# Optimization experiments

Measured on AMD Instinct MI355X. Metric: run time of the kernel, lower is better.

## Reference

```python
import jax, jax.numpy as jnp
from jax import lax
import numpy as np

B, T, C = 8, 16384, 64
NUM_FILTERS, FILTER_SIZE = 64, 5
LEAKY_SLOPE = 0.3  # keras activation 'leaky_relu' default negative_slope


def setup_inputs() -> dict:
    key = jax.random.key(0)
    k1, k2, k3 = jax.random.split(key, 3)
    x = jax.random.normal(k1, (B, T, C), dtype=jnp.float32)
    interp_weights = jax.random.normal(k2, (C,), dtype=jnp.float32)
    # Conv1D kernel layout: [filter_size, in_channels, out_channels]
    conv_kernel = jax.random.normal(k3, (FILTER_SIZE, C, NUM_FILTERS), dtype=jnp.float32) * 0.05
    conv_bias = jnp.zeros((NUM_FILTERS,), dtype=jnp.float32)
    return {"x": x, "interp_weights": interp_weights,
            "conv_kernel": conv_kernel, "conv_bias": conv_bias}


def reference(x, interp_weights, conv_kernel, conv_bias):
    # Sigmoid gate per channel
    w = jax.nn.sigmoid(interp_weights)  # [C]
    # The diag conv2d (filter [1,2,C,C], SAME) is: blend[t] = w*x[t] + (1-w)*x[t+1]
    # (TF SAME for even width pads one zero frame on the right)
    x_next = jnp.concatenate([x[:, 1:, :], jnp.zeros_like(x[:, :1, :])], axis=1)
    blend = w * x + (1.0 - w) * x_next  # [B, T, C]
    # Interleave: even positions original, odd positions blended -> [B, 2T, C]
    up = jnp.stack([x, blend], axis=2).reshape(B, 2 * T, C)
    # Conv1D(num_filters, filter_size, padding='same', stride 1) + leaky_relu
    y = lax.conv_general_dilated(
        up, conv_kernel,
        window_strides=(1,), padding='SAME',
        dimension_numbers=('NWC', 'WIO', 'NWC'))
    y = y + conv_bias
    return jnp.where(y >= 0, y, LEAKY_SLOPE * y)
```

## Files before the change

### kernel.cpp

```cpp
#include <hip/hip_runtime.h>
#include <hip/hip_bf16.h>
#include <cstdint>


#define T_ 16384
#define TWO_T 32768
#define XSTRIDE 72
#define WSL 1376

typedef __bf16 bf16x8 __attribute__((ext_vector_type(8)));
typedef __bf16 bf16x4 __attribute__((ext_vector_type(4)));
typedef float  f32x4  __attribute__((ext_vector_type(4)));
typedef unsigned short u16x8 __attribute__((ext_vector_type(8)));

__device__ __forceinline__ float sigmoidf_(float z) {
    return 1.0f / (1.0f + expf(-z));
}

__device__ __forceinline__ unsigned short f2bf(float f) {
    union { float f; uint32_t u; } v; v.f = f;
    uint32_t u = v.u;
    return (unsigned short)((u + 0x7FFFu + ((u >> 16) & 1u)) >> 16);
}

__global__ void lu_prep_kernel(const float* __restrict__ iw,
                               const float* __restrict__ ck,
                               const float* __restrict__ x,
                               unsigned short* __restrict__ bp,
                               float* __restrict__ corrf) {
    int fi = blockIdx.x;
    int l  = threadIdx.x;
    if (fi < 56) {
        int phase, ks, nt;
        if (fi < 24) { phase = 0; ks = fi >> 2; nt = fi & 3; }
        else         { phase = 1; ks = (fi - 24) >> 2; nt = (fi - 24) & 3; }
        int tap = ks >> 1;
        int n   = nt * 16 + (l & 15);
        int c0  = ((ks & 1) << 5) + ((l >> 4) << 3);
        u16x8 pk;
#pragma unroll
        for (int i = 0; i < 8; ++i) {
            int c = c0 + i;
            float w = sigmoidf_(iw[c]);
            float v;
            #define CK(k) ck[((k) * 64 + c) * 64 + n]
            if (phase == 0) {
                if (tap == 0)      v = CK(0) + w * CK(1);
                else if (tap == 1) v = (1.f - w) * CK(1) + CK(2) + w * CK(3);
                else               v = (1.f - w) * CK(3) + CK(4);
            } else {
                if (tap == 0)      v = w * CK(0);
                else if (tap == 1) v = (1.f - w) * CK(0) + CK(1) + w * CK(2);
                else if (tap == 2) v = (1.f - w) * CK(2) + CK(3) + w * CK(4);
                else               v = (1.f - w) * CK(4);
            }
            #undef CK
            pk[i] = f2bf(v);
        }
        *(u16x8*)(bp + (((size_t)fi * 64) + l) * 8) = pk;
    } else {
        int b = fi - 56;
        int f = l;
        float cE = 0.f, cO = 0.f;
#pragma unroll
        for (int c = 0; c < 64; ++c) {
            float w = sigmoidf_(iw[c]);
            float g = (1.f - w) * x[(size_t)b * T_ * 64 + c];
            cE += ck[(64 + c) * 64 + f] * g;
            cO += ck[c * 64 + f] * g;
        }
        corrf[b * 128 + f]      = cE;
        corrf[b * 128 + 64 + f] = cO;
    }
}

__device__ __forceinline__ void issue_loads(const float* __restrict__ x,
                                            int b, int t0, int lane, float4* ld) {
#pragma unroll
    for (int it = 0; it < 5; ++it) {
        int idx = it * 64 + lane;
        int j   = idx >> 4;
        int c4  = (idx & 15) << 2;
        int gf  = t0 - 1 + j;
        float4 v = make_float4(0.f, 0.f, 0.f, 0.f);
        if (idx < 304 && gf >= 0 && gf < T_)
            v = *(const float4*)(x + ((size_t)b * T_ + gf) * 64 + c4);
        ld[it] = v;
    }
}

__global__ __launch_bounds__(256, 4) void lu_main_kernel(
        const float* __restrict__ x,
        const unsigned short* __restrict__ bp,
        const float* __restrict__ corrf,
        const float* __restrict__ bias,
        float* __restrict__ out) {
    __shared__ __align__(16) unsigned short xl[4][WSL];

    const int bid  = blockIdx.x;
    const int b    = bid >> 8;
    const int p0   = (bid & 255) << 6;
    const int tid  = threadIdx.x;
    const int lane = tid & 63;
    const int wv   = tid >> 6;

    unsigned short* xw = &xl[wv][0];

    float4 ld[5];
    issue_loads(x, b, p0, lane, ld);

    bf16x8 We[6], Wo[8];
#pragma unroll
    for (int ks = 0; ks < 6; ++ks)
        We[ks] = __builtin_bit_cast(bf16x8,
            *(const u16x8*)(bp + (((size_t)(ks * 4 + wv)) * 64 + lane) * 8));
#pragma unroll
    for (int ks = 0; ks < 8; ++ks)
        Wo[ks] = __builtin_bit_cast(bf16x8,
            *(const u16x8*)(bp + (((size_t)(24 + ks * 4 + wv)) * 64 + lane) * 8));

    const int hi  = lane >> 4;
    const int col = lane & 15;
    const float4 bias4 = *(const float4*)(bias + (wv << 4) + (hi << 2));

    for (int w = 0; w < 4; ++w) {
        const int t0 = p0 + (w << 4);

#pragma unroll
        for (int it = 0; it < 5; ++it) {
            int idx = it * 64 + lane;
            if (idx < 304) {
                int j  = idx >> 4;
                int c4 = (idx & 15) << 2;
                bf16x4 pk;
                pk[0] = (__bf16)ld[it].x; pk[1] = (__bf16)ld[it].y;
                pk[2] = (__bf16)ld[it].z; pk[3] = (__bf16)ld[it].w;
                *(bf16x4*)(xw + j * XSTRIDE + c4) = pk;
            }
        }

        if (w < 3) issue_loads(x, b, p0 + ((w + 1) << 4), lane, ld);

        f32x4 accE = {0.f, 0.f, 0.f, 0.f};
        f32x4 accO = {0.f, 0.f, 0.f, 0.f};
#pragma unroll
        for (int tap = 0; tap < 4; ++tap)
#pragma unroll
            for (int h = 0; h < 2; ++h) {
                bf16x8 xb = __builtin_bit_cast(bf16x8,
                    *(const u16x8*)(xw + (col + tap) * XSTRIDE + (h << 5) + (hi << 3)));
                int ks = tap * 2 + h;
                if (tap < 3)
                    accE = __builtin_amdgcn_mfma_f32_16x16x32_bf16(We[ks], xb, accE, 0, 0, 0);
                accO = __builtin_amdgcn_mfma_f32_16x16x32_bf16(Wo[ks], xb, accO, 0, 0, 0);
            }

        if (((bid & 255) | w) == 0 && col == 0) {
            const float4 cE4 = *(const float4*)(corrf + b * 128 + (wv << 4) + (hi << 2));
            const float4 cO4 = *(const float4*)(corrf + b * 128 + 64 + (wv << 4) + (hi << 2));
            accE[0] -= cE4.x; accE[1] -= cE4.y; accE[2] -= cE4.z; accE[3] -= cE4.w;
            accO[0] -= cO4.x; accO[1] -= cO4.y; accO[2] -= cO4.z; accO[3] -= cO4.w;
        }

        const int tl = t0 + col;
        const size_t fbase = ((size_t)b * TWO_T + ((size_t)tl << 1)) * 64
                           + (wv << 4) + (hi << 2);
        float4 vE, vO;
        {
            float e0 = accE[0] + bias4.x, e1 = accE[1] + bias4.y,
                  e2 = accE[2] + bias4.z, e3 = accE[3] + bias4.w;
            vE.x = e0 >= 0.f ? e0 : 0.3f * e0;
            vE.y = e1 >= 0.f ? e1 : 0.3f * e1;
            vE.z = e2 >= 0.f ? e2 : 0.3f * e2;
            vE.w = e3 >= 0.f ? e3 : 0.3f * e3;
            float o0 = accO[0] + bias4.x, o1 = accO[1] + bias4.y,
                  o2 = accO[2] + bias4.z, o3 = accO[3] + bias4.w;
            vO.x = o0 >= 0.f ? o0 : 0.3f * o0;
            vO.y = o1 >= 0.f ? o1 : 0.3f * o1;
            vO.z = o2 >= 0.f ? o2 : 0.3f * o2;
            vO.w = o3 >= 0.f ? o3 : 0.3f * o3;
        }
        *(float4*)(out + fbase)      = vE;
        *(float4*)(out + fbase + 64) = vO;
    }
}

extern "C" void kernel_launch(void* const* d_in, const int* in_sizes, int n_in,
                              void* d_out, int out_size, void* d_ws, size_t ws_size,
                              hipStream_t stream) {
    (void)in_sizes; (void)n_in; (void)out_size; (void)ws_size;
    const float* x    = (const float*)d_in[0];
    const float* iw   = (const float*)d_in[1];
    const float* ck   = (const float*)d_in[2];
    const float* bias = (const float*)d_in[3];
    float* out = (float*)d_out;
    unsigned short* bp = (unsigned short*)d_ws;
    float* corrf = (float*)((char*)d_ws + 57344);

    lu_prep_kernel<<<64, 64, 0, stream>>>(iw, ck, x, bp, corrf);
    lu_main_kernel<<<2048, 256, 0, stream>>>(x, bp, corrf, bias, out);
}
```

Before: 34.53 us.

## Use LDS ring buffer with double-buffered prefetch and larger per-block tiles

Each wave now keeps a 32-row circular LDS buffer of bf16 x rows. Only the 16 new rows per step are loaded and converted, instead of reloading the 19-row halo window every step. Loads are double-buffered two steps ahead, and each block handles 128 time steps rather than 64, so the grid is halved. This cuts redundant global loads and conversions and gives more latency hiding, but uses more registers and leaves half as many blocks to spread across the GPU.

```diff
diff --git a/kernel.cpp b/kernel.cpp
--- a/kernel.cpp
+++ b/kernel.cpp
@@ -6,7 +6,7 @@
 #define T_ 16384
 #define TWO_T 32768
 #define XSTRIDE 72
-#define WSL 1376
+#define RING 32
 
 typedef __bf16 bf16x8 __attribute__((ext_vector_type(8)));
 typedef __bf16 bf16x4 __attribute__((ext_vector_type(4)));
@@ -74,18 +74,18 @@
     }
 }
 
-__device__ __forceinline__ void issue_loads(const float* __restrict__ x,
-                                            int b, int t0, int lane, float4* ld) {
-#pragma unroll
-    for (int it = 0; it < 5; ++it) {
-        int idx = it * 64 + lane;
+__device__ __forceinline__ void issue16(const float* __restrict__ xb,
+                                        int f0, int lane, float4* ld) {
+#pragma unroll
+    for (int i = 0; i < 4; ++i) {
+        int idx = i * 64 + lane;
         int j   = idx >> 4;
         int c4  = (idx & 15) << 2;
-        int gf  = t0 - 1 + j;
+        int gf  = f0 + j;
         float4 v = make_float4(0.f, 0.f, 0.f, 0.f);
-        if (idx < 304 && gf >= 0 && gf < T_)
-            v = *(const float4*)(x + ((size_t)b * T_ + gf) * 64 + c4);
-        ld[it] = v;
+        if (gf < T_)
+            v = *(const float4*)(xb + (size_t)gf * 64 + c4);
+        ld[i] = v;
     }
 }
 
@@ -95,19 +95,28 @@
         const float* __restrict__ corrf,
         const float* __restrict__ bias,
         float* __restrict__ out) {
-    __shared__ __align__(16) unsigned short xl[4][WSL];
+    __shared__ __align__(16) unsigned short xl[4][RING * XSTRIDE];
 
     const int bid  = blockIdx.x;
-    const int b    = bid >> 8;
-    const int p0   = (bid & 255) << 6;
-    const int tid  = threadIdx.x;
-    const int lane = tid & 63;
-    const int wv   = tid >> 6;
+    const int b    = bid >> 7;
+    const int q    = bid & 127;
+    const int p0   = q << 7;
+    const int lane = threadIdx.x & 63;
+    const int wv   = threadIdx.x >> 6;
 
     unsigned short* xw = &xl[wv][0];
-
-    float4 ld[5];
-    issue_loads(x, b, p0, lane, ld);
+    const float* xb = x + (size_t)b * T_ * 64;
+
+    float4 pro = make_float4(0.f, 0.f, 0.f, 0.f);
+    {
+        int j = lane >> 4, c4 = (lane & 15) << 2;
+        int gf = p0 - 1 + j;
+        if (lane < 48 && gf >= 0)
+            pro = *(const float4*)(xb + (size_t)gf * 64 + c4);
+    }
+    float4 ldb[2][4];
+    issue16(xb, p0 + 2,  lane, ldb[0]);
+    issue16(xb, p0 + 18, lane, ldb[1]);
 
     bf16x8 We[6], Wo[8];
 #pragma unroll
@@ -123,46 +132,57 @@
     const int col = lane & 15;
     const float4 bias4 = *(const float4*)(bias + (wv << 4) + (hi << 2));
 
-    for (int w = 0; w < 4; ++w) {
-        const int t0 = p0 + (w << 4);
-
-#pragma unroll
-        for (int it = 0; it < 5; ++it) {
-            int idx = it * 64 + lane;
-            if (idx < 304) {
-                int j  = idx >> 4;
-                int c4 = (idx & 15) << 2;
-                bf16x4 pk;
-                pk[0] = (__bf16)ld[it].x; pk[1] = (__bf16)ld[it].y;
-                pk[2] = (__bf16)ld[it].z; pk[3] = (__bf16)ld[it].w;
-                *(bf16x4*)(xw + j * XSTRIDE + c4) = pk;
-            }
-        }
-
-        if (w < 3) issue_loads(x, b, p0 + ((w + 1) << 4), lane, ld);
+    if (lane < 48) {
+        int j = lane >> 4, c4 = (lane & 15) << 2;
+        int r = (j + 31) & 31;
+        bf16x4 pk;
+        pk[0] = (__bf16)pro.x; pk[1] = (__bf16)pro.y;
+        pk[2] = (__bf16)pro.z; pk[3] = (__bf16)pro.w;
+        *(bf16x4*)(xw + r * XSTRIDE + c4) = pk;
+    }
+
+#pragma unroll
+    for (int w = 0; w < 8; ++w) {
+        const int par = w & 1;
+
+#pragma unroll
+        for (int i = 0; i < 4; ++i) {
+            int idx = i * 64 + lane;
+            int j   = idx >> 4;
+            int c4  = (idx & 15) << 2;
+            int r   = (16 * w + 2 + j) & 31;
+            bf16x4 pk;
+            pk[0] = (__bf16)ldb[par][i].x; pk[1] = (__bf16)ldb[par][i].y;
+            pk[2] = (__bf16)ldb[par][i].z; pk[3] = (__bf16)ldb[par][i].w;
+            *(bf16x4*)(xw + r * XSTRIDE + c4) = pk;
+        }
+
+        if (w < 6) issue16(xb, p0 + 16 * (w + 2) + 2, lane, ldb[par]);
 
         f32x4 accE = {0.f, 0.f, 0.f, 0.f};
         f32x4 accO = {0.f, 0.f, 0.f, 0.f};
 #pragma unroll
-        for (int tap = 0; tap < 4; ++tap)
+        for (int tap = 0; tap < 4; ++tap) {
+            const int r = (16 * w - 1 + col + tap) & 31;
 #pragma unroll
             for (int h = 0; h < 2; ++h) {
-                bf16x8 xb = __builtin_bit_cast(bf16x8,
-                    *(const u16x8*)(xw + (col + tap) * XSTRIDE + (h << 5) + (hi << 3)));
+                bf16x8 xfr = __builtin_bit_cast(bf16x8,
+                    *(const u16x8*)(xw + r * XSTRIDE + (h << 5) + (hi << 3)));
                 int ks = tap * 2 + h;
                 if (tap < 3)
-                    accE = __builtin_amdgcn_mfma_f32_16x16x32_bf16(We[ks], xb, accE, 0, 0, 0);
-                accO = __builtin_amdgcn_mfma_f32_16x16x32_bf16(Wo[ks], xb, accO, 0, 0, 0);
+                    accE = __builtin_amdgcn_mfma_f32_16x16x32_bf16(We[ks], xfr, accE, 0, 0, 0);
+                accO = __builtin_amdgcn_mfma_f32_16x16x32_bf16(Wo[ks], xfr, accO, 0, 0, 0);
             }
-
-        if (((bid & 255) | w) == 0 && col == 0) {
+        }
+
+        if (((q | w) == 0) && col == 0) {
             const float4 cE4 = *(const float4*)(corrf + b * 128 + (wv << 4) + (hi << 2));
             const float4 cO4 = *(const float4*)(corrf + b * 128 + 64 + (wv << 4) + (hi << 2));
             accE[0] -= cE4.x; accE[1] -= cE4.y; accE[2] -= cE4.z; accE[3] -= cE4.w;
             accO[0] -= cO4.x; accO[1] -= cO4.y; accO[2] -= cO4.z; accO[3] -= cO4.w;
         }
 
-        const int tl = t0 + col;
+        const int tl = p0 + (w << 4) + col;
         const size_t fbase = ((size_t)b * TWO_T + ((size_t)tl << 1)) * 64
                            + (wv << 4) + (hi << 2);
         float4 vE, vO;
@@ -198,5 +218,5 @@
     float* corrf = (float*)((char*)d_ws + 57344);
 
     lu_prep_kernel<<<64, 64, 0, stream>>>(iw, ck, x, bp, corrf);
-    lu_main_kernel<<<2048, 256, 0, stream>>>(x, bp, corrf, bias, out);
-}
+    lu_main_kernel<<<1024, 256, 0, stream>>>(x, bp, corrf, bias, out);
+}
```

Result: slower. 53.42 us (+54.7%).

## Stage input frames via direct global-to-LDS loads into swizzled fp32 ring buffer

Applied to the files above, without the earlier changes.

Replaces the register-staged load, bf16 convert and LDS write with global_load_lds DMA into a per-wave fp32 ring buffer using an XOR swizzle, with explicit vmcnt waits to overlap later loads with the MFMA work. Out-of-range frames read from a zeroed workspace page instead of being predicated. The bf16 conversion moves to after the LDS read, so LDS traffic doubles and the hand-tuned vmcnt counts depend on exact instruction ordering, which risks stalls or races.

```diff
diff --git a/kernel.cpp b/kernel.cpp
--- a/kernel.cpp
+++ b/kernel.cpp
@@ -5,11 +5,9 @@
 
 #define T_ 16384
 #define TWO_T 32768
-#define XSTRIDE 72
-#define WSL 1376
+#define RING 40
 
 typedef __bf16 bf16x8 __attribute__((ext_vector_type(8)));
-typedef __bf16 bf16x4 __attribute__((ext_vector_type(4)));
 typedef float  f32x4  __attribute__((ext_vector_type(4)));
 typedef unsigned short u16x8 __attribute__((ext_vector_type(8)));
 
@@ -27,7 +25,8 @@
                                const float* __restrict__ ck,
                                const float* __restrict__ x,
                                unsigned short* __restrict__ bp,
-                               float* __restrict__ corrf) {
+                               float* __restrict__ corrf,
+                               float* __restrict__ zp) {
     int fi = blockIdx.x;
     int l  = threadIdx.x;
     if (fi < 56) {
@@ -71,22 +70,35 @@
         }
         corrf[b * 128 + f]      = cE;
         corrf[b * 128 + 64 + f] = cO;
+        if (fi == 63) zp[l] = 0.f;
     }
 }
 
-__device__ __forceinline__ void issue_loads(const float* __restrict__ x,
-                                            int b, int t0, int lane, float4* ld) {
-#pragma unroll
-    for (int it = 0; it < 5; ++it) {
-        int idx = it * 64 + lane;
-        int j   = idx >> 4;
-        int c4  = (idx & 15) << 2;
-        int gf  = t0 - 1 + j;
-        float4 v = make_float4(0.f, 0.f, 0.f, 0.f);
-        if (idx < 304 && gf >= 0 && gf < T_)
-            v = *(const float4*)(x + ((size_t)b * T_ + gf) * 64 + c4);
-        ld[it] = v;
-    }
+__device__ __forceinline__ void gload16(const float* g, float* l) {
+    __builtin_amdgcn_global_load_lds(
+        (const __attribute__((address_space(1))) uint32_t*)g,
+        (__attribute__((address_space(3))) uint32_t*)l, 16, 0, 0);
+}
+
+__device__ __forceinline__ void stage4(const float* __restrict__ xb,
+                                       const float* __restrict__ zp,
+                                       int p0, int S, int lane, float* xw) {
+    int fr = S + (lane >> 4);
+    int f  = p0 + fr - 1;
+    int ch = (lane & 15) ^ ((fr - 1) & 7);
+    const float* gp = ((unsigned)f < (unsigned)T_)
+                    ? xb + ((size_t)f << 6) + (ch << 2)
+                    : zp + (ch << 2);
+    gload16(gp, xw + ((S % RING) << 6));
+}
+
+__device__ __forceinline__ bf16x8 pack8(f32x4 a, f32x4 b) {
+    bf16x8 r;
+    r[0] = (__bf16)a[0]; r[1] = (__bf16)a[1];
+    r[2] = (__bf16)a[2]; r[3] = (__bf16)a[3];
+    r[4] = (__bf16)b[0]; r[5] = (__bf16)b[1];
+    r[6] = (__bf16)b[2]; r[7] = (__bf16)b[3];
+    return r;
 }
 
 __global__ __launch_bounds__(256, 4) void lu_main_kernel(
@@ -94,20 +106,19 @@
         const unsigned short* __restrict__ bp,
         const float* __restrict__ corrf,
         const float* __restrict__ bias,
+        const float* __restrict__ zp,
         float* __restrict__ out) {
-    __shared__ __align__(16) unsigned short xl[4][WSL];
+    __shared__ __align__(16) float xl[4][RING * 64];
 
     const int bid  = blockIdx.x;
     const int b    = bid >> 8;
-    const int p0   = (bid & 255) << 6;
-    const int tid  = threadIdx.x;
-    const int lane = tid & 63;
-    const int wv   = tid >> 6;
-
-    unsigned short* xw = &xl[wv][0];
-
-    float4 ld[5];
-    issue_loads(x, b, p0, lane, ld);
+    const int q    = bid & 255;
+    const int p0   = q << 6;
+    const int lane = threadIdx.x & 63;
+    const int wv   = threadIdx.x >> 6;
+
+    float* xw = &xl[wv][0];
+    const float* xb = x + (size_t)b * T_ * 64;
 
     bf16x8 We[6], Wo[8];
 #pragma unroll
@@ -119,50 +130,58 @@
         Wo[ks] = __builtin_bit_cast(bf16x8,
             *(const u16x8*)(bp + (((size_t)(24 + ks * 4 + wv)) * 64 + lane) * 8));
 
-    const int hi  = lane >> 4;
-    const int col = lane & 15;
+    const int hi   = lane >> 4;
+    const int hi2  = hi << 1;
+    const int col  = lane & 15;
     const float4 bias4 = *(const float4*)(bias + (wv << 4) + (hi << 2));
-
+    const char* xwb = (const char*)xw;
+
+#pragma unroll
+    for (int k = 0; k < 5; ++k) stage4(xb, zp, p0, k * 4, lane, xw);
+
+#pragma unroll
     for (int w = 0; w < 4; ++w) {
-        const int t0 = p0 + (w << 4);
-
-#pragma unroll
-        for (int it = 0; it < 5; ++it) {
-            int idx = it * 64 + lane;
-            if (idx < 304) {
-                int j  = idx >> 4;
-                int c4 = (idx & 15) << 2;
-                bf16x4 pk;
-                pk[0] = (__bf16)ld[it].x; pk[1] = (__bf16)ld[it].y;
-                pk[2] = (__bf16)ld[it].z; pk[3] = (__bf16)ld[it].w;
-                *(bf16x4*)(xw + j * XSTRIDE + c4) = pk;
-            }
-        }
-
-        if (w < 3) issue_loads(x, b, p0 + ((w + 1) << 4), lane, ld);
+        if (w < 3) {
+#pragma unroll
+            for (int k = 0; k < 4; ++k)
+                stage4(xb, zp, p0, 20 + (w << 4) + (k << 2), lane, xw);
+        }
+
+        if (w == 0)      asm volatile("s_waitcnt vmcnt(4)" ::: "memory");
+        else if (w < 3)  asm volatile("s_waitcnt vmcnt(6)" ::: "memory");
+        else             asm volatile("s_waitcnt vmcnt(2)" ::: "memory");
+        __builtin_amdgcn_sched_barrier(0);
 
         f32x4 accE = {0.f, 0.f, 0.f, 0.f};
         f32x4 accO = {0.f, 0.f, 0.f, 0.f};
 #pragma unroll
-        for (int tap = 0; tap < 4; ++tap)
-#pragma unroll
-            for (int h = 0; h < 2; ++h) {
-                bf16x8 xb = __builtin_bit_cast(bf16x8,
-                    *(const u16x8*)(xw + (col + tap) * XSTRIDE + (h << 5) + (hi << 3)));
-                int ks = tap * 2 + h;
-                if (tap < 3)
-                    accE = __builtin_amdgcn_mfma_f32_16x16x32_bf16(We[ks], xb, accE, 0, 0, 0);
-                accO = __builtin_amdgcn_mfma_f32_16x16x32_bf16(Wo[ks], xb, accO, 0, 0, 0);
+        for (int tap = 0; tap < 4; ++tap) {
+            int fr  = (w << 4) + col + tap;
+            int row = fr - (fr >= RING ? RING : 0);
+            int key = (fr - 1) & 7;
+            int off0 = (row << 8) + ((hi2 ^ key) << 4);
+            f32x4 qa = *(const f32x4*)(xwb + off0);
+            f32x4 qb = *(const f32x4*)(xwb + (off0 ^ 16));
+            f32x4 qc = *(const f32x4*)(xwb + off0 + 128);
+            f32x4 qd = *(const f32x4*)(xwb + ((off0 + 128) ^ 16));
+            bf16x8 x0 = pack8(qa, qb);
+            bf16x8 x1 = pack8(qc, qd);
+            if (tap < 3) {
+                accE = __builtin_amdgcn_mfma_f32_16x16x32_bf16(We[tap * 2],     x0, accE, 0, 0, 0);
+                accE = __builtin_amdgcn_mfma_f32_16x16x32_bf16(We[tap * 2 + 1], x1, accE, 0, 0, 0);
             }
-
-        if (((bid & 255) | w) == 0 && col == 0) {
+            accO = __builtin_amdgcn_mfma_f32_16x16x32_bf16(Wo[tap * 2],     x0, accO, 0, 0, 0);
+            accO = __builtin_amdgcn_mfma_f32_16x16x32_bf16(Wo[tap * 2 + 1], x1, accO, 0, 0, 0);
+        }
+
+        if (((q | w) == 0) && col == 0) {
             const float4 cE4 = *(const float4*)(corrf + b * 128 + (wv << 4) + (hi << 2));
             const float4 cO4 = *(const float4*)(corrf + b * 128 + 64 + (wv << 4) + (hi << 2));
             accE[0] -= cE4.x; accE[1] -= cE4.y; accE[2] -= cE4.z; accE[3] -= cE4.w;
             accO[0] -= cO4.x; accO[1] -= cO4.y; accO[2] -= cO4.z; accO[3] -= cO4.w;
         }
 
-        const int tl = t0 + col;
+        const int tl = p0 + (w << 4) + col;
         const size_t fbase = ((size_t)b * TWO_T + ((size_t)tl << 1)) * 64
                            + (wv << 4) + (hi << 2);
         float4 vE, vO;
@@ -196,7 +215,8 @@
     float* out = (float*)d_out;
     unsigned short* bp = (unsigned short*)d_ws;
     float* corrf = (float*)((char*)d_ws + 57344);
-
-    lu_prep_kernel<<<64, 64, 0, stream>>>(iw, ck, x, bp, corrf);
-    lu_main_kernel<<<2048, 256, 0, stream>>>(x, bp, corrf, bias, out);
-}
+    float* zp    = (float*)((char*)d_ws + 61440);
+
+    lu_prep_kernel<<<64, 64, 0, stream>>>(iw, ck, x, bp, corrf, zp);
+    lu_main_kernel<<<2048, 256, 0, stream>>>(x, bp, corrf, bias, zp, out);
+}
```

After: 33.22 us. -3.8%, faster.

## Share one LDS tile of x across all waves, reload weights per step

Applied to the files above, without the earlier changes.

Before, each wave staged its own overlapping 19-frame window of x per 16-step chunk, with software-prefetched loads into registers. Now the whole block cooperatively loads and converts a single 67-frame bf16 tile into shared memory once, followed by one barrier. The per-wave weight fragments are no longer held in registers across iterations; they are reloaded from global/L1 inside each step, with an asm barrier to stop hoisting. Occupancy is raised to 8 blocks per CU. This removes redundant halo loads and register pressure, at the cost of losing load/compute overlap and adding repeated weight reads from cache.

```diff
diff --git a/kernel.cpp b/kernel.cpp
--- a/kernel.cpp
+++ b/kernel.cpp
@@ -5,8 +5,8 @@
 
 #define T_ 16384
 #define TWO_T 32768
+#define NFR 67
 #define XSTRIDE 72
-#define WSL 1376
 
 typedef __bf16 bf16x8 __attribute__((ext_vector_type(8)));
 typedef __bf16 bf16x4 __attribute__((ext_vector_type(4)));
@@ -74,95 +74,84 @@
     }
 }
 
-__device__ __forceinline__ void issue_loads(const float* __restrict__ x,
-                                            int b, int t0, int lane, float4* ld) {
-#pragma unroll
-    for (int it = 0; it < 5; ++it) {
-        int idx = it * 64 + lane;
-        int j   = idx >> 4;
-        int c4  = (idx & 15) << 2;
-        int gf  = t0 - 1 + j;
-        float4 v = make_float4(0.f, 0.f, 0.f, 0.f);
-        if (idx < 304 && gf >= 0 && gf < T_)
-            v = *(const float4*)(x + ((size_t)b * T_ + gf) * 64 + c4);
-        ld[it] = v;
-    }
-}
-
-__global__ __launch_bounds__(256, 4) void lu_main_kernel(
+__global__ __launch_bounds__(256, 8) void lu_main_kernel(
         const float* __restrict__ x,
         const unsigned short* __restrict__ bp,
         const float* __restrict__ corrf,
         const float* __restrict__ bias,
         float* __restrict__ out) {
-    __shared__ __align__(16) unsigned short xl[4][WSL];
+    __shared__ __align__(16) unsigned short xl[NFR * XSTRIDE];
 
     const int bid  = blockIdx.x;
     const int b    = bid >> 8;
-    const int p0   = (bid & 255) << 6;
+    const int q    = bid & 255;
+    const int p0   = q << 6;
     const int tid  = threadIdx.x;
     const int lane = tid & 63;
     const int wv   = tid >> 6;
 
-    unsigned short* xw = &xl[wv][0];
+    const float* xb = x + (size_t)b * T_ * 64;
 
-    float4 ld[5];
-    issue_loads(x, b, p0, lane, ld);
-
-    bf16x8 We[6], Wo[8];
 #pragma unroll
-    for (int ks = 0; ks < 6; ++ks)
-        We[ks] = __builtin_bit_cast(bf16x8,
-            *(const u16x8*)(bp + (((size_t)(ks * 4 + wv)) * 64 + lane) * 8));
-#pragma unroll
-    for (int ks = 0; ks < 8; ++ks)
-        Wo[ks] = __builtin_bit_cast(bf16x8,
-            *(const u16x8*)(bp + (((size_t)(24 + ks * 4 + wv)) * 64 + lane) * 8));
+    for (int it = 0; it < 5; ++it) {
+        int idx = it * 256 + tid;
+        if (idx < NFR * 16) {
+            int j  = idx >> 4;
+            int c4 = (idx & 15) << 2;
+            int gf = p0 - 1 + j;
+            float4 v = make_float4(0.f, 0.f, 0.f, 0.f);
+            if ((unsigned)gf < (unsigned)T_)
+                v = *(const float4*)(xb + ((size_t)gf << 6) + c4);
+            bf16x4 pk;
+            pk[0] = (__bf16)v.x; pk[1] = (__bf16)v.y;
+            pk[2] = (__bf16)v.z; pk[3] = (__bf16)v.w;
+            *(bf16x4*)(xl + j * XSTRIDE + c4) = pk;
+        }
+    }
 
     const int hi  = lane >> 4;
     const int col = lane & 15;
     const float4 bias4 = *(const float4*)(bias + (wv << 4) + (hi << 2));
 
+    __syncthreads();
+
+#pragma unroll 1
     for (int w = 0; w < 4; ++w) {
-        const int t0 = p0 + (w << 4);
-
-#pragma unroll
-        for (int it = 0; it < 5; ++it) {
-            int idx = it * 64 + lane;
-            if (idx < 304) {
-                int j  = idx >> 4;
-                int c4 = (idx & 15) << 2;
-                bf16x4 pk;
-                pk[0] = (__bf16)ld[it].x; pk[1] = (__bf16)ld[it].y;
-                pk[2] = (__bf16)ld[it].z; pk[3] = (__bf16)ld[it].w;
-                *(bf16x4*)(xw + j * XSTRIDE + c4) = pk;
-            }
-        }
-
-        if (w < 3) issue_loads(x, b, p0 + ((w + 1) << 4), lane, ld);
+        uint64_t bpa = (uint64_t)bp;
+        asm("" : "+v"(bpa));
+        const unsigned short* bpw = (const unsigned short*)bpa;
 
         f32x4 accE = {0.f, 0.f, 0.f, 0.f};
         f32x4 accO = {0.f, 0.f, 0.f, 0.f};
 #pragma unroll
-        for (int tap = 0; tap < 4; ++tap)
-#pragma unroll
-            for (int h = 0; h < 2; ++h) {
-                bf16x8 xb = __builtin_bit_cast(bf16x8,
-                    *(const u16x8*)(xw + (col + tap) * XSTRIDE + (h << 5) + (hi << 3)));
-                int ks = tap * 2 + h;
-                if (tap < 3)
-                    accE = __builtin_amdgcn_mfma_f32_16x16x32_bf16(We[ks], xb, accE, 0, 0, 0);
-                accO = __builtin_amdgcn_mfma_f32_16x16x32_bf16(Wo[ks], xb, accO, 0, 0, 0);
+        for (int tap = 0; tap < 4; ++tap) {
+            int r = (w << 4) + col + tap;
+            bf16x8 x0 = __builtin_bit_cast(bf16x8,
+                *(const u16x8*)(xl + r * XSTRIDE + (hi << 3)));
+            bf16x8 x1 = __builtin_bit_cast(bf16x8,
+                *(const u16x8*)(xl + r * XSTRIDE + 32 + (hi << 3)));
+            const size_t f0 = (size_t)(((tap * 2) * 4 + wv) * 64 + lane) * 8;
+            const size_t f1 = (size_t)(((tap * 2 + 1) * 4 + wv) * 64 + lane) * 8;
+            if (tap < 3) {
+                bf16x8 we0 = __builtin_bit_cast(bf16x8, *(const u16x8*)(bpw + f0));
+                bf16x8 we1 = __builtin_bit_cast(bf16x8, *(const u16x8*)(bpw + f1));
+                accE = __builtin_amdgcn_mfma_f32_16x16x32_bf16(we0, x0, accE, 0, 0, 0);
+                accE = __builtin_amdgcn_mfma_f32_16x16x32_bf16(we1, x1, accE, 0, 0, 0);
             }
+            bf16x8 wo0 = __builtin_bit_cast(bf16x8, *(const u16x8*)(bpw + f0 + 12288));
+            bf16x8 wo1 = __builtin_bit_cast(bf16x8, *(const u16x8*)(bpw + f1 + 12288));
+            accO = __builtin_amdgcn_mfma_f32_16x16x32_bf16(wo0, x0, accO, 0, 0, 0);
+            accO = __builtin_amdgcn_mfma_f32_16x16x32_bf16(wo1, x1, accO, 0, 0, 0);
+        }
 
-        if (((bid & 255) | w) == 0 && col == 0) {
+        if (((q | w) == 0) && col == 0) {
             const float4 cE4 = *(const float4*)(corrf + b * 128 + (wv << 4) + (hi << 2));
             const float4 cO4 = *(const float4*)(corrf + b * 128 + 64 + (wv << 4) + (hi << 2));
             accE[0] -= cE4.x; accE[1] -= cE4.y; accE[2] -= cE4.z; accE[3] -= cE4.w;
             accO[0] -= cO4.x; accO[1] -= cO4.y; accO[2] -= cO4.z; accO[3] -= cO4.w;
         }
 
-        const int tl = t0 + col;
+        const int tl = p0 + (w << 4) + col;
         const size_t fbase = ((size_t)b * TWO_T + ((size_t)tl << 1)) * 64
                            + (wv << 4) + (hi << 2);
         float4 vE, vO;
```

Measured after the change: 43.06 us. 1.25x slower.
